# Optimization experiments

Measured on AMD Instinct MI355X. Metric: run time of the kernel, lower is better.

## Reference

```python
import jax, jax.numpy as jnp
import numpy as np

N, TX, TZ, DX, DZ, DATT, DOUT = 8, 2048, 2048, 1024, 1024, 1024, 1024


def setup_inputs() -> dict:
    key = jax.random.key(0)
    ks = jax.random.split(key, 8)
    s = 0.02
    x = jax.random.normal(ks[0], (N, TX, DX), dtype=jnp.float32)
    z = jax.random.normal(ks[1], (N, TZ, DZ), dtype=jnp.float32)
    Wq = jax.random.normal(ks[2], (DX, DATT), dtype=jnp.float32) * s
    bq = jnp.zeros((DATT,), dtype=jnp.float32)
    Wk = jax.random.normal(ks[3], (DZ, DATT), dtype=jnp.float32) * s
    bk = jnp.zeros((DATT,), dtype=jnp.float32)
    Wv = jax.random.normal(ks[4], (DZ, DOUT), dtype=jnp.float32) * s
    bv = jnp.zeros((DOUT,), dtype=jnp.float32)
    # fixed boolean mask [Tx, Tz]; causal lower-triangular so no row is fully masked
    mask = jnp.tril(jnp.ones((TX, TZ), dtype=bool))
    return {"x": x, "z": z, "Wq": Wq, "bq": bq, "Wk": Wk, "bk": bk,
            "Wv": Wv, "bv": bv, "mask": mask}


def reference(x, z, Wq, bq, Wk, bk, Wv, bv, mask):
    Datt = Wq.shape[1]
    Q = x @ Wq + bq                      # [N, Tx, Datt]
    K = z @ Wk + bk                      # [N, Tz, Datt]
    V = z @ Wv + bv                      # [N, Tz, Dout]
    S = jnp.einsum('bxd,bzd->bxz', Q, K)  # [N, Tx, Tz]
    S = jnp.where(mask[None, :, :], S, -jnp.inf)
    A = jax.nn.softmax(S / jnp.sqrt(jnp.float32(Datt)), axis=-1)
    y = jnp.einsum('bxz,bzo->bxo', A, V)  # [N, Tx, Dout]
    return y
```

## Files before the change

### kernel.cpp

```cpp
#include <hip/hip_runtime.h>

typedef _Float16 f16;
typedef _Float16 f16x8 __attribute__((ext_vector_type(8)));
typedef _Float16 f16x4 __attribute__((ext_vector_type(4)));
typedef float    f32x4 __attribute__((ext_vector_type(4)));

constexpr int NB   = 8;
constexpr int T    = 2048;
constexpr int D    = 1024;
constexpr int NTRI = 136;

__device__ __forceinline__ void load_lds16(const f16* g, f16* l) {
    __builtin_amdgcn_global_load_lds(
        (const __attribute__((address_space(1))) void*)g,
        (__attribute__((address_space(3))) void*)l, 16, 0, 0);
}

__global__ __launch_bounds__(256) void cast_transpose_w(
    const float* __restrict__ W0, const float* __restrict__ W1,
    const float* __restrict__ W2, f16* __restrict__ Wt)
{
    __shared__ f16 tile[32][33];
    const int which = blockIdx.z;
    const float* W = which == 0 ? W0 : (which == 1 ? W1 : W2);
    f16* dst = Wt + (size_t)which * D * D;
    const int c0 = blockIdx.x * 32, r0 = blockIdx.y * 32;
    const int tx = threadIdx.x & 31, ty = threadIdx.x >> 5;
    #pragma unroll
    for (int i = 0; i < 32; i += 8)
        tile[ty + i][tx] = (f16)W[(size_t)(r0 + ty + i) * D + c0 + tx];
    __syncthreads();
    #pragma unroll
    for (int i = 0; i < 32; i += 8)
        dst[(size_t)(c0 + ty + i) * D + r0 + tx] = tile[tx][ty + i];
}

__global__ __launch_bounds__(256) void cast_xz(
    const float* __restrict__ x, const float* __restrict__ z,
    f16* __restrict__ xh, f16* __restrict__ zh)
{
    const float* src = blockIdx.y ? z : x;
    f16* dst = blockIdx.y ? zh : xh;
    const size_t i = ((size_t)blockIdx.x * 256 + threadIdx.x) * 4;
    const float4 v = *(const float4*)(src + i);
    f16x4 u = { (f16)v.x, (f16)v.y, (f16)v.z, (f16)v.w };
    *(f16x4*)(dst + i) = u;
}

template<int MODE>
__global__ __launch_bounds__(256) void gemm_nt(
    const f16* __restrict__ Ag_, const f16* __restrict__ Bg_,
    void* __restrict__ Cg_, void* __restrict__ Cg2_,
    const float* __restrict__ bias, const float* __restrict__ bias2,
    float* __restrict__ rsum)
{
    __shared__ f16 As[2 * 128 * 32];
    __shared__ f16 Bs[2 * 128 * 32];

    int bx, by;
    const int bz = blockIdx.z;
    if (MODE == 1) {
        const int idx = blockIdx.x;
        by = (int)((sqrtf(8.0f * idx + 1.0f) - 1.0f) * 0.5f);
        while ((by + 1) * (by + 2) / 2 <= idx) ++by;
        while (by * (by + 1) / 2 > idx) --by;
        bx = idx - by * (by + 1) / 2;
    } else if (MODE == 2) {
        bx = blockIdx.x; by = 15 - blockIdx.y;
    } else {
        bx = blockIdx.x; by = blockIdx.y;
    }

    const size_t bm0 = (size_t)by * 128, bn0 = (size_t)bx * 128;
    const f16* Abase; const f16* Bbase;
    int lda, ldb, K;
    if (MODE == 0 || MODE == 4) {
        Abase = Ag_ + bm0 * D;                       lda = D;
        Bbase = Bg_ + bn0 * D;                       ldb = D; K = D;
    } else if (MODE == 1) {
        Abase = Ag_ + (size_t)bz * T * D + bm0 * D;  lda = D;
        Bbase = Bg_ + (size_t)bz * T * D + bn0 * D;  ldb = D; K = D;
    } else {
        Abase = Ag_ + ((size_t)bz * NTRI + (size_t)by * (by + 1) / 2) * 16384;
        lda = 128;
        Bbase = Bg_ + (size_t)bz * D * T + bn0 * T;  ldb = T;
        K = (by + 1) * 128;
    }

    const int t    = threadIdx.x;
    const int lane = t & 63, wave = t >> 6;
    const int wr   = (wave >> 1) * 64, wc = (wave & 1) * 64;
    const int fr   = lane & 15, fo = (lane >> 4) * 8;
    const int srow = t >> 2;
    const int scol = (t & 3) * 8;
    const int wub  = (t & 192) * 8;

    f32x4 acc[4][4] = {};

    for (int k0 = 0; k0 < K; k0 += 64) {
        #pragma unroll
        for (int p = 0; p < 2; ++p) {
            const int k = k0 + p * 32;
            const f16* Ak;
            if (MODE == 2) Ak = Abase + (size_t)(k >> 7) * 16384 + (k & 127);
            else           Ak = Abase + k;
            #pragma unroll
            for (int it = 0; it < 2; ++it)
                load_lds16(Ak + (size_t)(it * 64 + srow) * lda + scol,
                           As + p * 4096 + it * 2048 + wub);
            #pragma unroll
            for (int it = 0; it < 2; ++it)
                load_lds16(Bbase + k + (size_t)(it * 64 + srow) * ldb + scol,
                           Bs + p * 4096 + it * 2048 + wub);
        }
        __syncthreads();

        #pragma unroll
        for (int p = 0; p < 2; ++p) {
            f16x8 av[4], bv[4];
            #pragma unroll
            for (int i = 0; i < 4; ++i)
                av[i] = *(const f16x8*)&As[p * 4096 + (wr + i * 16 + fr) * 32 + fo];
            #pragma unroll
            for (int j = 0; j < 4; ++j)
                bv[j] = *(const f16x8*)&Bs[p * 4096 + (wc + j * 16 + fr) * 32 + fo];
            #pragma unroll
            for (int i = 0; i < 4; ++i)
                #pragma unroll
                for (int j = 0; j < 4; ++j)
                    acc[i][j] = __builtin_amdgcn_mfma_f32_16x16x32_f16(av[i], bv[j], acc[i][j], 0, 0, 0);
        }
        __syncthreads();
    }

    const int cr = (lane >> 4) * 4, cc = lane & 15;
    if (MODE == 0) {
        f16* Cp = (f16*)Cg_;
        #pragma unroll
        for (int j = 0; j < 4; ++j) {
            const int col = (int)bn0 + wc + j * 16 + cc;
            const float bb = bias[col];
            #pragma unroll
            for (int i = 0; i < 4; ++i)
                #pragma unroll
                for (int g = 0; g < 4; ++g)
                    Cp[(bm0 + wr + i * 16 + cr + g) * D + col] = (f16)(acc[i][j][g] + bb);
        }
    } else if (MODE == 4) {
        if (bx < 8) {
            f16* Cp = (f16*)Cg_;
            #pragma unroll
            for (int j = 0; j < 4; ++j) {
                const int col = (int)bn0 + wc + j * 16 + cc;
                const float bb = bias[col];
                #pragma unroll
                for (int i = 0; i < 4; ++i)
                    #pragma unroll
                    for (int g = 0; g < 4; ++g)
                        Cp[(bm0 + wr + i * 16 + cr + g) * D + col] = (f16)(acc[i][j][g] + bb);
            }
        } else {
            f16* Vt = (f16*)Cg2_;
            const int b  = (int)(bm0 >> 11);
            const int r0 = (int)(bm0 & 2047);
            #pragma unroll
            for (int j = 0; j < 4; ++j) {
                const int colv = (int)bn0 - 1024 + wc + j * 16 + cc;
                const float bb = bias2[colv];
                #pragma unroll
                for (int i = 0; i < 4; ++i) {
                    f16x4 pk = { (f16)(acc[i][j][0] + bb), (f16)(acc[i][j][1] + bb),
                                 (f16)(acc[i][j][2] + bb), (f16)(acc[i][j][3] + bb) };
                    *(f16x4*)&Vt[(size_t)b * D * T + (size_t)colv * T + r0 + wr + i * 16 + cr] = pk;
                }
            }
        }
    } else if (MODE == 1) {
        f16* Cp = (f16*)Cg_ + ((size_t)bz * NTRI + (size_t)by * (by + 1) / 2 + bx) * 16384;
        float* rs = rsum + (size_t)bz * T + bm0;
        float rowsum[4][4] = {};
        #pragma unroll
        for (int i = 0; i < 4; ++i)
            #pragma unroll
            for (int j = 0; j < 4; ++j)
                #pragma unroll
                for (int g = 0; g < 4; ++g) {
                    const int lr = wr + i * 16 + cr + g, lc = wc + j * 16 + cc;
                    const int r = (int)bm0 + lr, c = (int)bn0 + lc;
                    const float p = (c > r) ? 0.0f : __expf(acc[i][j][g] * 0.03125f);
                    Cp[lr * 128 + lc] = (f16)p;
                    rowsum[i][g] += p;
                }
        #pragma unroll
        for (int i = 0; i < 4; ++i)
            #pragma unroll
            for (int g = 0; g < 4; ++g) {
                float s = rowsum[i][g];
                s += __shfl_xor(s, 1, 64);
                s += __shfl_xor(s, 2, 64);
                s += __shfl_xor(s, 4, 64);
                s += __shfl_xor(s, 8, 64);
                if (cc == 0) atomicAdd(&rs[wr + i * 16 + cr + g], s);
            }
    } else {
        float* Cp = (float*)Cg_ + (size_t)bz * T * D;
        const float* rs = rsum + (size_t)bz * T;
        #pragma unroll
        for (int i = 0; i < 4; ++i) {
            const int r4 = (int)bm0 + wr + i * 16 + cr;
            float rinv[4];
            #pragma unroll
            for (int g = 0; g < 4; ++g) rinv[g] = 1.0f / rs[r4 + g];
            #pragma unroll
            for (int j = 0; j < 4; ++j)
                #pragma unroll
                for (int g = 0; g < 4; ++g)
                    Cp[(size_t)(r4 + g) * D + bn0 + wc + j * 16 + cc] = acc[i][j][g] * rinv[g];
        }
    }
}

extern "C" void kernel_launch(void* const* d_in, const int* in_sizes, int n_in,
                              void* d_out, int out_size, void* d_ws, size_t ws_size,
                              hipStream_t stream)
{
    const float* x  = (const float*)d_in[0];
    const float* z  = (const float*)d_in[1];
    const float* Wq = (const float*)d_in[2];
    const float* bq = (const float*)d_in[3];
    const float* Wk = (const float*)d_in[4];
    const float* bk = (const float*)d_in[5];
    const float* Wv = (const float*)d_in[6];
    const float* bv = (const float*)d_in[7];
    float* out = (float*)d_out;

    char* ws = (char*)d_ws;
    f16*   Wt   = (f16*)(ws);
    f16*   xh   = (f16*)(ws + 6291456ull);
    f16*   zh   = (f16*)(ws + 39845888ull);
    f16*   Qh   = (f16*)(ws + 73400320ull);
    f16*   Kh   = (f16*)(ws + 106954752ull);
    f16*   Vt   = (f16*)(ws + 140509184ull);
    f16*   SA   = (f16*)(ws + 174063616ull);
    float* rsum = (float*)(ws + 209715200ull);

    hipMemsetAsync(rsum, 0, (size_t)NB * T * sizeof(float), stream);
    cast_transpose_w<<<dim3(32, 32, 3), 256, 0, stream>>>(Wq, Wk, Wv, Wt);
    cast_xz<<<dim3(16384, 2, 1), 256, 0, stream>>>(x, z, xh, zh);
    gemm_nt<0><<<dim3(8, 128, 1), 256, 0, stream>>>(xh, Wt, Qh, nullptr, bq, nullptr, nullptr);
    gemm_nt<4><<<dim3(16, 128, 1), 256, 0, stream>>>(zh, Wt + 1048576, Kh, Vt, bk, bv, nullptr);
    gemm_nt<1><<<dim3(136, 1, 8), 256, 0, stream>>>(Qh, Kh, SA, nullptr, nullptr, nullptr, rsum);
    gemm_nt<2><<<dim3(8, 16, 8), 256, 0, stream>>>(SA, Vt, out, nullptr, nullptr, nullptr, rsum);
}
```

Before: 497.0 us.

## Double-buffer GEMM K-loop, XOR-swizzle LDS layout, and remap block order for L2 locality

The GEMM K-loop becomes a software pipeline over 32-wide K stages. The next stage's global-to-LDS loads are issued before computing on the current buffer, so loads overlap MFMA work, and there is one barrier per stage instead of two per 64-wide step. The LDS columns are XOR-swizzled on both the store and the fragment-read side to reduce bank conflicts. For the non-triangular modes, block IDs are remapped in strided groups of eight so that concurrently running blocks share operand tiles in cache. The remap assumes a fixed grid shape of 128 rows and 8 or 16 columns. Removing the second barrier relies on the async LDS loads landing safely in the other buffer.

Result: slower. 553.1 us (+11.3%).

```diff
diff --git a/kernel.cpp b/kernel.cpp
--- a/kernel.cpp
+++ b/kernel.cpp
@@ -68,7 +68,13 @@
     } else if (MODE == 2) {
         bx = blockIdx.x; by = 15 - blockIdx.y;
     } else {
-        bx = blockIdx.x; by = blockIdx.y;
+        constexpr int GX  = (MODE == 0) ? 8 : 16;
+        constexpr int LGX = (MODE == 0) ? 3 : 4;
+        constexpr int NWG = GX * 128;
+        int id = (int)blockIdx.y * GX + (int)blockIdx.x;
+        id = (id & 7) * (NWG >> 3) + (id >> 3);
+        bx = id & (GX - 1);
+        by = id >> LGX;
     }
 
     const size_t bm0 = (size_t)by * 128, bn0 = (size_t)bx * 128;
@@ -92,44 +98,50 @@
     const int wr   = (wave >> 1) * 64, wc = (wave & 1) * 64;
     const int fr   = lane & 15, fo = (lane >> 4) * 8;
     const int srow = t >> 2;
-    const int scol = (t & 3) * 8;
+    const int scol = ((t & 3) ^ ((t >> 2) & 3)) * 8;
     const int wub  = (t & 192) * 8;
+    const int fsw  = fo ^ ((fr & 3) << 3);
+    const int arow = (wr + fr) * 32 + fsw;
+    const int brow = (wc + fr) * 32 + fsw;
 
     f32x4 acc[4][4] = {};
-
-    for (int k0 = 0; k0 < K; k0 += 64) {
-        #pragma unroll
-        for (int p = 0; p < 2; ++p) {
-            const int k = k0 + p * 32;
-            const f16* Ak;
-            if (MODE == 2) Ak = Abase + (size_t)(k >> 7) * 16384 + (k & 127);
-            else           Ak = Abase + k;
-            #pragma unroll
-            for (int it = 0; it < 2; ++it)
-                load_lds16(Ak + (size_t)(it * 64 + srow) * lda + scol,
-                           As + p * 4096 + it * 2048 + wub);
-            #pragma unroll
-            for (int it = 0; it < 2; ++it)
-                load_lds16(Bbase + k + (size_t)(it * 64 + srow) * ldb + scol,
-                           Bs + p * 4096 + it * 2048 + wub);
-        }
-        __syncthreads();
-
-        #pragma unroll
-        for (int p = 0; p < 2; ++p) {
-            f16x8 av[4], bv[4];
-            #pragma unroll
-            for (int i = 0; i < 4; ++i)
-                av[i] = *(const f16x8*)&As[p * 4096 + (wr + i * 16 + fr) * 32 + fo];
+    const int nk = K >> 5;
+
+    auto stage = [&](int s, int b) {
+        const int k = s * 32;
+        const f16* Ak;
+        if (MODE == 2) Ak = Abase + (size_t)(k >> 7) * 16384 + (k & 127);
+        else           Ak = Abase + k;
+        #pragma unroll
+        for (int it = 0; it < 2; ++it)
+            load_lds16(Ak + (size_t)(it * 64 + srow) * lda + scol,
+                       As + b * 4096 + it * 2048 + wub);
+        #pragma unroll
+        for (int it = 0; it < 2; ++it)
+            load_lds16(Bbase + k + (size_t)(it * 64 + srow) * ldb + scol,
+                       Bs + b * 4096 + it * 2048 + wub);
+    };
+
+    stage(0, 0);
+    __syncthreads();
+
+    for (int s = 0; s < nk; ++s) {
+        const int cur = s & 1;
+        if (s + 1 < nk) stage(s + 1, cur ^ 1);
+
+        f16x8 av[4], bv[4];
+        #pragma unroll
+        for (int i = 0; i < 4; ++i)
+            av[i] = *(const f16x8*)&As[cur * 4096 + arow + i * 512];
+        #pragma unroll
+        for (int j = 0; j < 4; ++j)
+            bv[j] = *(const f16x8*)&Bs[cur * 4096 + brow + j * 512];
+        #pragma unroll
+        for (int i = 0; i < 4; ++i)
             #pragma unroll
             for (int j = 0; j < 4; ++j)
-                bv[j] = *(const f16x8*)&Bs[p * 4096 + (wc + j * 16 + fr) * 32 + fo];
-            #pragma unroll
-            for (int i = 0; i < 4; ++i)
-                #pragma unroll
-                for (int j = 0; j < 4; ++j)
-                    acc[i][j] = __builtin_amdgcn_mfma_f32_16x16x32_f16(av[i], bv[j], acc[i][j], 0, 0, 0);
-        }
+                acc[i][j] = __builtin_amdgcn_mfma_f32_16x16x32_f16(av[i], bv[j], acc[i][j], 0, 0, 0);
+
         __syncthreads();
     }
 
```
